# Kernel optimization log

Hardware: AMD Instinct MI355X
Metric: run time of the kernel (lower is better)

## Reference

```python
import jax, jax.numpy as jnp
from jax import lax
import numpy as np

# HH / synapse constants (CFG in original repo; standard values matching the rate eqns)
GNA, GK, GL = 40.0, 35.0, 0.3
ENA, EK, EL = 55.0, -77.0, -65.0
GS, VS = 1.0, 0.0
IAPP = 1.0
VT, KP = -20.0, 3.0
A_D, A_R = 1.0, 0.1
DT = 0.02

B, N, L = 16, 2000, 1024


def setup_inputs() -> dict:
    key = jax.random.key(0)
    z = jax.random.uniform(key, (B, N, L), dtype=jnp.float32)
    return {"z": z}


def _rates(V):
    # Singularity-safe rate constants (the torch code patches V==25 / V==-35 exactly).
    at25 = V == 25.0
    atm35 = V == -35.0
    dN = jnp.where(at25, 1.0, 1.0 - jnp.exp((-V + 25.0) / 9.0))
    dM = jnp.where(atm35, 1.0, 1.0 - jnp.exp((-V - 35.0) / 9.0))
    dNb = jnp.where(at25, 1.0, 1.0 - jnp.exp((V - 25.0) / 9.0))
    dMb = jnp.where(atm35, 1.0, 1.0 - jnp.exp((V + 35.0) / 9.0))
    aN = jnp.where(at25, 0.18, 0.02 * (V - 25.0) / dN)
    bN = jnp.where(at25, 0.08, -0.002 * (V - 25.0) / dNb)
    aM = jnp.where(atm35, 1.638, 0.182 * (V + 35.0) / dM)
    bM = jnp.where(atm35, 1.16, -0.124 * (V + 35.0) / dMb)
    aH = 0.25 * jnp.exp((-V - 90.0) / 12.0)
    bH = 0.25 * jnp.exp((V + 34.0) / 12.0)
    return aN, bN, aM, bM, aH, bH


def _step(carry, z_prev):
    V, m, n, h, y = carry
    pow1 = GNA * m ** 3 * h
    pow2 = GK * n ** 4
    G = DT / 2 * (pow1 + pow2 + GL + GS * y)
    E = pow1 * ENA + pow2 * EK + GL * EL + GS * VS * y
    Vn = (V * (1.0 - G) + DT * (E + IAPP)) / (1.0 + G)
    aN, bN, aM, bM, aH, bH = _rates(Vn)
    mn = (aM * DT + (1.0 - DT / 2 * (aM + bM)) * m) / (DT / 2 * (aM + bM) + 1.0)
    nn = (aN * DT + (1.0 - DT / 2 * (aN + bN)) * n) / (DT / 2 * (aN + bN) + 1.0)
    hn = (aH * DT + (1.0 - DT / 2 * (aH + bH)) * h) / (DT / 2 * (aH + bH) + 1.0)
    ady = A_D * z_prev
    yn = (ady * DT + (1.0 - DT / 2 * (ady + A_R)) * y) / (DT / 2 * (ady + A_R) + 1.0)
    return (Vn, mn, nn, hn, yn), Vn


def _hh(z):
    b, n_t, l = z.shape
    zt = jnp.moveaxis(z, 1, 0)  # (N, B, L); step k uses z[k-1]
    V0 = jnp.full((b, l), -70.0, dtype=z.dtype)
    zeros = jnp.zeros((b, l), dtype=z.dtype)
    ones = jnp.ones((b, l), dtype=z.dtype)
    carry0 = (V0, zeros, zeros, ones, zeros)
    _, Vseq = lax.scan(_step, carry0, zt[:-1])  # (N-1, B, L)
    Vall = jnp.concatenate([V0[None], Vseq], axis=0)  # (N, B, L)
    V = jnp.moveaxis(Vall, 0, 1)  # (B, N, L)
    return jax.nn.sigmoid((V - VT) / KP)


def reference(z):
    return _hh(z)
```

## Files before the change

### kernel.cpp

```cpp
#include <hip/hip_runtime.h>

#define N_ 2000
#define L_ 1024

__device__ __forceinline__ float rcpf(float d) { return __builtin_amdgcn_rcpf(d); }
__device__ __forceinline__ float ex2(float x)  { return __builtin_amdgcn_exp2f(x); }

#define STEP1(K, RS)                                                          \
  {                                                                           \
    const int kk = (K);                                                       \
    float zc = zb[RS];                                                        \
    int kpre = kk + 7;                                                        \
    int kc = kpre < 1998 ? kpre : 1998;                                       \
    zb[RS] = z[base + kc * L_];                                               \
     \
    float m2   = m * m;                                                       \
    float m3   = m2 * m;                                                      \
    float valm = m3 * h;                                           \
    float n2   = n * n;                                                       \
    float valn = n2 * n2;                                            \
    float gy   = __fmaf_rn(y, 0.01f, 0.003f);                                 \
    float G    = __fmaf_rn(valm, 0.4f, __fmaf_rn(valn, 0.35f, gy));           \
    float E    = __fmaf_rn(valm, 2200.0f, __fmaf_rn(valn, -2695.0f, -19.5f)); \
    float num  = __fmaf_rn(V, 1.0f - G, __fmaf_rn(E, 0.02f, 0.02f));          \
    float Vn   = num * rcpf(1.0f + G);                                        \
        \
    float eRm  = ex2(__fmaf_rn(Vn, K9, 35.0f * K9));                          \
    float um   = Vn + 35.0f;                                                  \
    float urm  = um * rcpf(eRm - 1.0f);                                       \
    bool  patm = (Vn == -35.0f);                                              \
    float aM   = patm ? 1.638f   : 0.182f * (urm * eRm);                      \
    float s1m  = patm ? 0.02798f : urm * __fmaf_rn(0.00182f, eRm, 0.00124f);  \
                                           \
    float eRn  = ex2(__fmaf_rn(Vn, K9, -25.0f * K9));                         \
    float un   = Vn - 25.0f;                                                  \
    float urn  = un * rcpf(eRn - 1.0f);                                       \
    bool  patn = (Vn == 25.0f);                                               \
    float aN   = patn ? 0.18f   : 0.02f * (urn * eRn);                        \
    float s1n  = patn ? 0.0026f : urn * __fmaf_rn(0.0002f, eRn, 0.00002f);    \
                                                                 \
    float aH   = 0.25f * ex2(__fmaf_rn(Vn, -K12, -90.0f * K12));              \
    float bH   = 0.25f * ex2(__fmaf_rn(Vn,  K12,  34.0f * K12));              \
                                                \
    float qm   = 1.0f + s1m;                                                  \
    float numm = __fmaf_rn(aM, 0.02f, __fmaf_rn(-s1m, m, m));                 \
    float qn   = 1.0f + s1n;                                                  \
    float numn = __fmaf_rn(aN, 0.02f, __fmaf_rn(-s1n, n, n));                 \
    float sh   = __fmaf_rn(aH, 0.01f, 0.01f * bH);                            \
    float qh   = 1.0f + sh;                                                   \
    float numh = __fmaf_rn(aH, 0.02f, __fmaf_rn(-sh, h, h));                  \
    float sy   = __fmaf_rn(zc, 0.01f, 0.001f);                                \
    float qy   = 1.0f + sy;                                                   \
    float numy = __fmaf_rn(zc, 0.02f, __fmaf_rn(-sy, y, y));                  \
    float rq1  = rcpf(qm * qh);                                               \
    m = numm * (rq1 * qh);                                                    \
    h = numh * (rq1 * qm);                                                    \
    float rq2  = rcpf(qn * qy);                                               \
    n = numn * (rq2 * qy);                                                    \
    y = numy * (rq2 * qn);                                                    \
    V = Vn;                                                                   \
                          \
    float e2 = eRm * eRm;                                                     \
    float ts = (e2 * eRm) * 0.006737946999085467f;                            \
    float sg = ts * rcpf(1.0f + ts);                                          \
    out[base + kk * L_] = sg;                                                 \
  }

__global__ __launch_bounds__(64) void hh_kernel(const float* __restrict__ z,
                                                float* __restrict__ out) {
    const int t   = blockIdx.x * 64 + threadIdx.x;
    const int b   = t >> 10;
    const int l   = t & 1023;
    const int base = b * (N_ * L_) + l;

    const float K9  = 0.16029944898766259f;
    const float K12 = 0.12022458674074695f;

    float V = -70.0f;
    float m = 0.0f, n = 0.0f, h = 1.0f, y = 0.0f;

    float zb[8];
#pragma unroll
    for (int i = 0; i < 8; ++i) zb[i] = z[base + i * L_];

    out[base] = 5.777750e-8f;

    int k = 1;
    for (int g = 0; g < 249; ++g) {
#pragma unroll
        for (int j = 0; j < 8; ++j) {
            STEP1(k + j, j)
        }
        k += 8;
    }
#pragma unroll
    for (int j = 0; j < 7; ++j) {
        STEP1(k + j, j)
    }
}

extern "C" void kernel_launch(void* const* d_in, const int* in_sizes, int n_in,
                              void* d_out, int out_size, void* d_ws, size_t ws_size,
                              hipStream_t stream) {
    const float* z = (const float*)d_in[0];
    float* out = (float*)d_out;
    hh_kernel<<<256, 64, 0, stream>>>(z, out);
}
```

Measured before the change: 510.2 us.

## Split each HH channel's gate updates across four lanes with DPP reductions

Each (batch, position) channel now occupies four adjacent lanes. Lanes handle the m, n, h and y gate updates respectively, so the serial per-step dependency chain shrinks per lane. G and E are reduced across the quad with DPP moves, and h is broadcast with DPP. The grid grows from 256 to 1024 blocks to fill more of the GPU, which the old 256 single-wave blocks left underused. The cost is redundant V computation in every lane, lane-divergent constants, DPP latency on the critical path, and z loads duplicated across the four lanes.

```diff
diff --git a/kernel.cpp b/kernel.cpp
--- a/kernel.cpp
+++ b/kernel.cpp
@@ -6,97 +6,124 @@
 __device__ __forceinline__ float rcpf(float d) { return __builtin_amdgcn_rcpf(d); }
 __device__ __forceinline__ float ex2(float x)  { return __builtin_amdgcn_exp2f(x); }
 
-#define STEP1(K, RS)                                                          \
+__device__ __forceinline__ float dpp_bcast2(float x) {
+    return __int_as_float(__builtin_amdgcn_mov_dpp(__float_as_int(x), 0xAA, 0xF, 0xF, true));
+}
+__device__ __forceinline__ float dpp_x1(float x) {
+    return __int_as_float(__builtin_amdgcn_mov_dpp(__float_as_int(x), 0xB1, 0xF, 0xF, true));
+}
+__device__ __forceinline__ float dpp_x2(float x) {
+    return __int_as_float(__builtin_amdgcn_mov_dpp(__float_as_int(x), 0x4E, 0xF, 0xF, true));
+}
+
+#define STEP1(RS, DOLOAD)                                                     \
   {                                                                           \
-    const int kk = (K);                                                       \
     float zc = zb[RS];                                                        \
-    int kpre = kk + 7;                                                        \
-    int kc = kpre < 1998 ? kpre : 1998;                                       \
-    zb[RS] = z[base + kc * L_];                                               \
-     \
-    float m2   = m * m;                                                       \
-    float m3   = m2 * m;                                                      \
-    float valm = m3 * h;                                           \
-    float n2   = n * n;                                                       \
-    float valn = n2 * n2;                                            \
-    float gy   = __fmaf_rn(y, 0.01f, 0.003f);                                 \
-    float G    = __fmaf_rn(valm, 0.4f, __fmaf_rn(valn, 0.35f, gy));           \
-    float E    = __fmaf_rn(valm, 2200.0f, __fmaf_rn(valn, -2695.0f, -19.5f)); \
-    float num  = __fmaf_rn(V, 1.0f - G, __fmaf_rn(E, 0.02f, 0.02f));          \
-    float Vn   = num * rcpf(1.0f + G);                                        \
-        \
-    float eRm  = ex2(__fmaf_rn(Vn, K9, 35.0f * K9));                          \
-    float um   = Vn + 35.0f;                                                  \
-    float urm  = um * rcpf(eRm - 1.0f);                                       \
-    bool  patm = (Vn == -35.0f);                                              \
-    float aM   = patm ? 1.638f   : 0.182f * (urm * eRm);                      \
-    float s1m  = patm ? 0.02798f : urm * __fmaf_rn(0.00182f, eRm, 0.00124f);  \
-                                           \
-    float eRn  = ex2(__fmaf_rn(Vn, K9, -25.0f * K9));                         \
-    float un   = Vn - 25.0f;                                                  \
-    float urn  = un * rcpf(eRn - 1.0f);                                       \
-    bool  patn = (Vn == 25.0f);                                               \
-    float aN   = patn ? 0.18f   : 0.02f * (urn * eRn);                        \
-    float s1n  = patn ? 0.0026f : urn * __fmaf_rn(0.0002f, eRn, 0.00002f);    \
-                                                                 \
-    float aH   = 0.25f * ex2(__fmaf_rn(Vn, -K12, -90.0f * K12));              \
-    float bH   = 0.25f * ex2(__fmaf_rn(Vn,  K12,  34.0f * K12));              \
-                                                \
-    float qm   = 1.0f + s1m;                                                  \
-    float numm = __fmaf_rn(aM, 0.02f, __fmaf_rn(-s1m, m, m));                 \
-    float qn   = 1.0f + s1n;                                                  \
-    float numn = __fmaf_rn(aN, 0.02f, __fmaf_rn(-s1n, n, n));                 \
-    float sh   = __fmaf_rn(aH, 0.01f, 0.01f * bH);                            \
-    float qh   = 1.0f + sh;                                                   \
-    float numh = __fmaf_rn(aH, 0.02f, __fmaf_rn(-sh, h, h));                  \
-    float sy   = __fmaf_rn(zc, 0.01f, 0.001f);                                \
-    float qy   = 1.0f + sy;                                                   \
-    float numy = __fmaf_rn(zc, 0.02f, __fmaf_rn(-sy, y, y));                  \
-    float rq1  = rcpf(qm * qh);                                               \
-    m = numm * (rq1 * qh);                                                    \
-    h = numh * (rq1 * qm);                                                    \
-    float rq2  = rcpf(qn * qy);                                               \
-    n = numn * (rq2 * qy);                                                    \
-    y = numy * (rq2 * qn);                                                    \
-    V = Vn;                                                                   \
-                          \
-    float e2 = eRm * eRm;                                                     \
-    float ts = (e2 * eRm) * 0.006737946999085467f;                            \
-    float sg = ts * rcpf(1.0f + ts);                                          \
-    out[base + kk * L_] = sg;                                                 \
+    if (DOLOAD) { zb[RS] = *zpre; zpre += L_; }                               \
+                                      \
+    float hX  = dpp_bcast2(st);                   \
+    float s2v = st * st;                                                      \
+    float v3h = (s2v * st) * hX;                         \
+    float v4  = s2v * s2v;                               \
+    float val = isM ? v3h : (isN ? v4 : st);                                  \
+    float gP  = __fmaf_rn(val, cg, cgad);                                     \
+    float eP  = __fmaf_rn(val, ce, cead);                                     \
+    gP += dpp_x1(gP); gP += dpp_x2(gP);            \
+    eP += dpp_x1(eP); eP += dpp_x2(eP);                                       \
+    float num = __fmaf_rn(V, 1.0f - gP, __fmaf_rn(eP, 0.02f, 0.02f));         \
+    float Vn  = num * rcpf(1.0f + gP);                                        \
+                 \
+    float eA  = ex2(__fmaf_rn(Vn, sA1, cA1));                                 \
+    float eB  = ex2(__fmaf_rn(Vn, sB1, cB1));            \
+    float rr  = rcpf(eA + cD);                        \
+    float u   = Vn + cu;                                                      \
+          \
+    float X    = __fmaf_rn(ks1, rr, ks0);                                     \
+    float sAux = __fmaf_rn(kse, eA + eB, cS);                                 \
+    sAux       = __fmaf_rn(zm01, zc, sAux);                                   \
+    float s    = __fmaf_rn(u, X, sAux);                                       \
+                                      \
+    float p   = kA * u;                                                       \
+    float aRw = __fmaf_rn(p, rr, p);                                          \
+    float a2  = __fmaf_rn(k2, eA, aRw);                                       \
+    a2        = __fmaf_rn(zm, zc, a2);                                        \
+    bool pat  = (Vn == cc);                      \
+    s  = pat ? pS : s;                                                        \
+    a2 = pat ? pA : a2;                                                       \
+                                                 \
+    float q    = 1.0f + s;                                                    \
+    float numr = __fmaf_rn(a2, 0.02f, __fmaf_rn(-s, st, st));                 \
+    st = numr * rcpf(q);                                                      \
+    V  = Vn;                                                                  \
+                             \
+    float sg = eA * rr;                                                       \
+    if (s3) *outp = sg;                                                       \
+    outp += L_;                                                               \
   }
 
 __global__ __launch_bounds__(64) void hh_kernel(const float* __restrict__ z,
                                                 float* __restrict__ out) {
     const int t   = blockIdx.x * 64 + threadIdx.x;
-    const int b   = t >> 10;
-    const int l   = t & 1023;
+    const int sub = t & 3;
+    const int ch  = t >> 2;
+    const int b   = ch >> 10;
+    const int l   = ch & 1023;
     const int base = b * (N_ * L_) + l;
+
+    const bool isM = (sub == 0);
+    const bool isN = (sub == 1);
+    const bool s3  = (sub == 3);
 
     const float K9  = 0.16029944898766259f;
     const float K12 = 0.12022458674074695f;
+    const float K3  = 0.48089834696298783f;
 
-    float V = -70.0f;
-    float m = 0.0f, n = 0.0f, h = 1.0f, y = 0.0f;
+    float sA1, cA1, sB1, cB1, cD, cu, kA, k2, zm, ks1, ks0, kse, cS, zm01;
+    float cg, cgad, ce, cead, cc, pA, pS;
+    if (sub == 0) {
+        sA1 = K9;   cA1 = 35.0f * K9;   sB1 = 0.0f; cB1 = 0.0f;
+        cD  = -1.0f; cu = 35.0f;  kA = 0.182f; k2 = 0.0f; zm = 0.0f;
+        ks1 = 0.00306f; ks0 = 0.00182f; kse = 0.0f; cS = 0.0f; zm01 = 0.0f;
+        cg = 0.40f; cgad = 0.0f;    ce = 2200.0f;  cead = 0.0f;
+        cc = -35.0f; pA = 1.638f; pS = 0.02798f;
+    } else if (sub == 1) {
+        sA1 = K9;   cA1 = -25.0f * K9;  sB1 = 0.0f; cB1 = 0.0f;
+        cD  = -1.0f; cu = -25.0f; kA = 0.02f;  k2 = 0.0f; zm = 0.0f;
+        ks1 = 0.00022f; ks0 = 0.0002f;  kse = 0.0f; cS = 0.0f; zm01 = 0.0f;
+        cg = 0.35f; cgad = 0.0f;    ce = -2695.0f; cead = 0.0f;
+        cc = 25.0f;  pA = 0.18f;  pS = 0.0026f;
+    } else if (sub == 2) {
+        sA1 = -K12; cA1 = -90.0f * K12; sB1 = K12;  cB1 = 34.0f * K12;
+        cD  = 1.0f;  cu = 0.0f;   kA = 0.0f;   k2 = 0.25f; zm = 0.0f;
+        ks1 = 0.0f; ks0 = 0.0f;  kse = 0.0025f; cS = 0.0f; zm01 = 0.0f;
+        cg = 0.0f;  cgad = 0.003f;  ce = 0.0f;     cead = -19.5f;
+        cc = 1e30f;  pA = 0.0f;   pS = 0.0f;
+    } else {
+        sA1 = K3;   cA1 = 20.0f * K3;   sB1 = 0.0f; cB1 = 0.0f;
+        cD  = 1.0f;  cu = 0.0f;   kA = 0.0f;   k2 = 0.0f;  zm = 1.0f;
+        ks1 = 0.0f; ks0 = 0.0f;  kse = 0.0f;    cS = 0.001f; zm01 = 0.01f;
+        cg = 0.01f; cgad = 0.0f;    ce = 0.0f;     cead = 0.0f;
+        cc = 1e30f;  pA = 0.0f;   pS = 0.0f;
+    }
+
+    float V  = -70.0f;
+    float st = (sub == 2) ? 1.0f : 0.0f;
 
     float zb[8];
+    const float* zp0 = z + base;
 #pragma unroll
-    for (int i = 0; i < 8; ++i) zb[i] = z[base + i * L_];
+    for (int i = 0; i < 8; ++i) zb[i] = zp0[i * L_];
+    const float* zpre = z + base + 8 * L_;
+    float* outp = out + base + L_;
 
-    out[base] = 5.777750e-8f;
+    if (s3) out[base] = 5.777750e-8f;
 
-    int k = 1;
     for (int g = 0; g < 249; ++g) {
 #pragma unroll
-        for (int j = 0; j < 8; ++j) {
-            STEP1(k + j, j)
-        }
-        k += 8;
+        for (int j = 0; j < 8; ++j) STEP1(j, true)
     }
 #pragma unroll
-    for (int j = 0; j < 7; ++j) {
-        STEP1(k + j, j)
-    }
+    for (int j = 0; j < 7; ++j) STEP1(j, false)
 }
 
 extern "C" void kernel_launch(void* const* d_in, const int* in_sizes, int n_in,
@@ -104,5 +131,5 @@
                               hipStream_t stream) {
     const float* z = (const float*)d_in[0];
     float* out = (float*)d_out;
-    hh_kernel<<<256, 64, 0, stream>>>(z, out);
+    hh_kernel<<<1024, 64, 0, stream>>>(z, out);
 }
```

Result: no change. 504.7 us (-1.1%).
